# Optimization experiments

Hardware: AMD Instinct MI355X
Metric: run time of the kernel (lower is better)

## Reference

```python
import jax, jax.numpy as jnp
import numpy as np

DIM = 512
HEADS = 1
DIM_HEAD = DIM // 8          # 64
M = DIM // 2                 # 256 landmarks
ITERS = 6                    # pinv iterations
SCALE = DIM_HEAD ** -0.5
KSIZE = 33                   # residual conv kernel (seq dim)
EPS_LN = 1e-5


def setup_inputs() -> dict:
    key = jax.random.key(0)
    ks = jax.random.split(key, 6)
    B, N = 4, 4096  # N multiple of M -> no padding branch
    return {
        "x": jax.random.normal(ks[0], (B, N, DIM), jnp.float32),
        "norm_gamma": jnp.ones((DIM,), jnp.float32),
        "norm_beta": jnp.zeros((DIM,), jnp.float32),
        "w_qkv": jax.random.normal(ks[1], (DIM, 3 * HEADS * DIM_HEAD), jnp.float32) * 0.02,
        "w_out": jax.random.normal(ks[2], (HEADS * DIM_HEAD, DIM), jnp.float32) * 0.02,
        "b_out": jnp.zeros((DIM,), jnp.float32),
        "w_conv": jax.random.normal(ks[3], (HEADS, 1, KSIZE, 1), jnp.float32) * 0.02,
    }


def _moore_penrose_pinv(x, iters=ITERS):
    # x: [B, H, M, M]
    abs_x = jnp.abs(x)
    col = abs_x.sum(-1)
    row = abs_x.sum(-2)
    z = jnp.swapaxes(x, -1, -2) / (jnp.max(col) * jnp.max(row))  # global maxes, as in torch
    I = jnp.eye(x.shape[-1], dtype=x.dtype)
    for _ in range(iters):
        xz = x @ z
        z = 0.25 * z @ (13.0 * I - xz @ (15.0 * I - xz @ (7.0 * I - xz)))
    return z


def reference(x, norm_gamma, norm_beta, w_qkv, w_out, b_out, w_conv):
    B, N, _ = x.shape
    # LayerNorm (biased variance, matches torch)
    mu = x.mean(-1, keepdims=True)
    var = x.var(-1, keepdims=True)
    xn = (x - mu) / jnp.sqrt(var + EPS_LN) * norm_gamma + norm_beta

    qkv = xn @ w_qkv  # [B, N, 3*H*D]
    q, k, v = jnp.split(qkv, 3, axis=-1)
    resh = lambda t: t.reshape(B, N, HEADS, DIM_HEAD).transpose(0, 2, 1, 3)  # [B,H,N,D]
    q, k, v = resh(q), resh(k), resh(v)
    q = q * SCALE

    # landmarks: mean of l=N/M consecutive tokens
    l = N // M
    q_l = q.reshape(B, HEADS, M, l, DIM_HEAD).sum(3) / l  # [B,H,M,D]
    k_l = k.reshape(B, HEADS, M, l, DIM_HEAD).sum(3) / l

    sim1 = jnp.einsum('bhnd,bhmd->bhnm', q, k_l)    # [B,H,N,M]
    sim2 = jnp.einsum('bhid,bhjd->bhij', q_l, k_l)  # [B,H,M,M]
    sim3 = jnp.einsum('bhmd,bhnd->bhmn', q_l, k)    # [B,H,M,N]
    a1 = jax.nn.softmax(sim1, axis=-1)
    a2 = jax.nn.softmax(sim2, axis=-1)
    a3 = jax.nn.softmax(sim3, axis=-1)

    a2_inv = _moore_penrose_pinv(a2)
    left = a1 @ a2_inv                      # [B,H,N,M]
    out = left @ (a3 @ v)                   # [B,H,N,D]

    # residual depthwise conv over the sequence dim (treat [N,D] as HxW image)
    res = jax.lax.conv_general_dilated(
        v, w_conv, window_strides=(1, 1),
        padding=((KSIZE // 2, KSIZE // 2), (0, 0)),
        dimension_numbers=('NCHW', 'OIHW', 'NCHW'),
        feature_group_count=HEADS)
    out = out + res

    out = out.transpose(0, 2, 1, 3).reshape(B, N, HEADS * DIM_HEAD)
    out = out @ w_out + b_out               # to_out (dropout is eval no-op)

    attn = left @ a3                        # full approx attention [B,H,N,N]
    return (x + out, attn)
```

## Files before the change

### kernel.cpp

```cpp
#include <hip/hip_runtime.h>
#include <hip/hip_bf16.h>


typedef _Float16 f16;
typedef f16 f16x2 __attribute__((ext_vector_type(2)));
typedef f16 f16x4 __attribute__((ext_vector_type(4)));
typedef f16 f16x8 __attribute__((ext_vector_type(8)));
typedef float f32x4 __attribute__((ext_vector_type(4)));

__device__ __forceinline__ float waveMax(float v){
  #pragma unroll
  for(int i=32;i>0;i>>=1) v = fmaxf(v, __shfl_xor(v, i));
  return v;
}
__device__ __forceinline__ float waveSum(float v){
  #pragma unroll
  for(int i=32;i>0;i>>=1) v += __shfl_xor(v, i);
  return v;
}
__device__ __forceinline__ float blockMaxF(float v, float* sm){
  v = waveMax(v);
  if((threadIdx.x&63)==0) sm[threadIdx.x>>6] = v;
  __syncthreads();
  v = fmaxf(fmaxf(sm[0],sm[1]), fmaxf(sm[2],sm[3]));
  __syncthreads();
  return v;
}
__device__ __forceinline__ float blockSumF(float v, float* sm){
  v = waveSum(v);
  if((threadIdx.x&63)==0) sm[threadIdx.x>>6] = v;
  __syncthreads();
  v = sm[0]+sm[1]+sm[2]+sm[3];
  __syncthreads();
  return v;
}

__device__ __forceinline__ void async_cp16(const f16* g, const f16* l){
  __builtin_amdgcn_global_load_lds((const __attribute__((address_space(1))) void*)g,
                                   (__attribute__((address_space(3))) void*)l, 16, 0, 0);
}

__device__ __forceinline__ void gemm_body(
    const f16* __restrict__ A, const f16* __restrict__ Bt, void* __restrict__ C, int cf16,
    int N, int K, int m0, int n0, int kt0, int ktn,
    const float* __restrict__ bias, const float* __restrict__ resid,
    f16* As, f16* Bs)
{
  int t = threadIdx.x;
  int w = t>>6, lane = t&63;
  int quad = lane>>4, l16 = lane&15;
  int wr = w>>1, wc = w&1;
  f32x4 acc[4][4] = {};
  for(int kt=kt0; kt<kt0+ktn; ++kt){
    #pragma unroll
    for(int i=0;i<4;++i){
      int G = (w<<8)+(i<<6)+lane;
      int row = G>>3, gs = G&7;
      int g = gs ^ (row&7);
      int koff = (kt<<6)+(g<<3);
      async_cp16(A + (long)(m0+row)*K + koff, As + (((w<<8)+(i<<6))<<3));
      async_cp16(Bt + (long)(n0+row)*K + koff, Bs + (((w<<8)+(i<<6))<<3));
    }
    __syncthreads();
    #pragma unroll
    for(int kk=0; kk<2; ++kk){
      f16x8 af[4], bfr[4];
      int gb = (kk<<2) + quad;
      #pragma unroll
      for(int mi=0;mi<4;++mi){
        int row = (wr<<6)+(mi<<4)+l16;
        af[mi] = *(const f16x8*)(As + ((row<<6) + ((gb ^ (row&7))<<3)));
      }
      #pragma unroll
      for(int ni=0;ni<4;++ni){
        int row = (wc<<6)+(ni<<4)+l16;
        bfr[ni] = *(const f16x8*)(Bs + ((row<<6) + ((gb ^ (row&7))<<3)));
      }
      #pragma unroll
      for(int mi=0;mi<4;++mi){
        #pragma unroll
        for(int ni=0;ni<4;++ni)
          acc[mi][ni] = __builtin_amdgcn_mfma_f32_16x16x32_f16(af[mi], bfr[ni], acc[mi][ni], 0,0,0);
      }
    }
    __syncthreads();
  }
  #pragma unroll
  for(int mi=0;mi<4;++mi){
    int rowb = m0 + (wr<<6) + (mi<<4) + (quad<<2);
    #pragma unroll
    for(int ni=0;ni<4;++ni){
      int col = n0 + (wc<<6) + (ni<<4) + l16;
      if(col < N){
        #pragma unroll
        for(int r=0;r<4;++r){
          float v = acc[mi][ni][r];
          if(bias)  v += bias[col];
          if(resid) v += resid[(long)(rowb+r)*N + col];
          if(cf16) ((f16*)C)[(long)(rowb+r)*N + col] = (f16)v;
          else     ((float*)C)[(long)(rowb+r)*N + col] = v;
        }
      }
    }
  }
}

__device__ __forceinline__ void g256_body(const float* __restrict__ A, const float* __restrict__ B,
    const float* __restrict__ E, float* __restrict__ D, int Ncols, float beta, float alpha,
    int AS, int BS, int ES, int bx, int by, int b, int ks, float* At, float* Bss, float diagv)
{
  long aOff = (long)b*65536;
  long bBatch = 256L*Ncols, bSl = 4L*bBatch;
  long bOff = (long)b*bBatch;
  long dOff = (long)ks*bSl + bOff;
  int r0 = bx*64, c0 = by*64;
  int t = threadIdx.x, tr = t>>4, tc = t&15;
  int arow = t>>2, ac4 = t&3;
  int bk = t>>4, bn4 = t&15;
  float acc[4][4] = {};
  for(int k0=ks*64;k0<ks*64+64;k0+=16){
    const float* pa = A + aOff + (long)(r0+arow)*256 + k0 + ac4*4;
    float4 va = *(const float4*)pa;
    for(int s=1;s<AS;++s){ float4 w2 = *(const float4*)(pa + (long)s*262144);
      va.x+=w2.x; va.y+=w2.y; va.z+=w2.z; va.w+=w2.w; }
    At[(ac4*4+0)*72+arow]=va.x; At[(ac4*4+1)*72+arow]=va.y;
    At[(ac4*4+2)*72+arow]=va.z; At[(ac4*4+3)*72+arow]=va.w;
    const float* pb = B + bOff + (long)(k0+bk)*Ncols + c0 + bn4*4;
    float4 vb = *(const float4*)pb;
    for(int s=1;s<BS;++s){ float4 w2 = *(const float4*)(pb + (long)s*bSl);
      vb.x+=w2.x; vb.y+=w2.y; vb.z+=w2.z; vb.w+=w2.w; }
    *(float4*)&Bss[bk*72+bn4*4] = vb;
    __syncthreads();
    #pragma unroll
    for(int kk=0;kk<16;++kk){
      float4 a4 = *(const float4*)&At[kk*72+tr*4];
      float4 b4 = *(const float4*)&Bss[kk*72+tc*4];
      float av[4] = {a4.x,a4.y,a4.z,a4.w};
      float bv[4] = {b4.x,b4.y,b4.z,b4.w};
      #pragma unroll
      for(int i=0;i<4;++i){
        #pragma unroll
        for(int j=0;j<4;++j) acc[i][j] += av[i]*bv[j];
      }
    }
    __syncthreads();
  }
  #pragma unroll
  for(int i=0;i<4;++i){
    int row = r0 + tr*4 + i;
    #pragma unroll
    for(int j=0;j<4;++j){
      int col = c0 + tc*4 + j;
      float v = beta*acc[i][j];
      if(ks==0){
        if(ES>0){
          const float* pe = E + aOff + (long)row*256 + col;
          float e = pe[0];
          for(int s=1;s<ES;++s) e += pe[(long)s*262144];
          v += alpha*e;
        }
        if(row==col) v += diagv;
      }
      D[dOff + (long)row*Ncols + col] = v;
    }
  }
}

__global__ __launch_bounds__(256) void k_ln_prep(const float* __restrict__ x, const float* __restrict__ g,
    const float* __restrict__ be, f16* __restrict__ xn, const float* __restrict__ wqkv,
    const float* __restrict__ wout, f16* __restrict__ wqkT, f16* __restrict__ woutT,
    float* __restrict__ rs, unsigned* __restrict__ csmax){
  __shared__ float sm[8];
  int blk = blockIdx.x; int t = threadIdx.x;
  if(blk < 16384){
    long row = blk;
    const float* xr = x + row*512;
    float v0 = xr[t], v1 = xr[t+256];
    float s = waveSum(v0+v1), ss = waveSum(v0*v0+v1*v1);
    if((t&63)==0){ sm[t>>6] = s; sm[(t>>6)+4] = ss; }
    __syncthreads();
    s = sm[0]+sm[1]+sm[2]+sm[3]; ss = sm[4]+sm[5]+sm[6]+sm[7];
    float mu = s*(1.f/512.f);
    float var = ss*(1.f/512.f) - mu*mu;
    float rstd = rsqrtf(var + 1e-5f);
    xn[row*512+t]     = (f16)((v0-mu)*rstd*g[t]     + be[t]);
    xn[row*512+t+256] = (f16)((v1-mu)*rstd*g[t+256] + be[t+256]);
  } else if(blk < 16896){
    int i = (blk-16384)*256 + t; int n = i>>9, k = i&511;
    wqkT[i] = (n<192) ? (f16)wqkv[k*192+n] : (f16)0.0f;
  } else if(blk < 17024){
    int i = (blk-16896)*256 + t; int n = i>>6, k = i&63;
    woutT[i] = (f16)wout[k*512+n];
  } else {
    rs[t]=0.f; rs[t+256]=0.f; rs[t+512]=0.f; rs[t+768]=0.f;
    if(t==0){ *csmax = 0u; }
  }
}

__global__ __launch_bounds__(256) void k_qkv(const f16* __restrict__ xn, const f16* __restrict__ wqkT,
                                             float* __restrict__ qkv){
  __shared__ f16 As[8192];
  __shared__ f16 Bs[8192];
  int blk = blockIdx.x;
  int bx = blk&127, by = blk>>7;
  gemm_body(xn, wqkT, qkv, 0, 192, 512, bx*128, by*128, 0, 8, nullptr, nullptr, As, Bs);
}

__global__ __launch_bounds__(256) void k_splitvl(const float* __restrict__ qkv,
    f16* __restrict__ qf, f16* __restrict__ kf, float* __restrict__ vf,
    f16* __restrict__ vT, f16* __restrict__ ql, f16* __restrict__ kl){
  __shared__ float tile[64][65];
  int blk = blockIdx.x; int t = threadIdx.x;
  if(blk < 4096){
    long row = (long)blk*4 + (t>>6); int d = t&63;
    const float* p = qkv + row*192;
    qf[row*64+d] = (f16)(p[d]*0.125f);
    kf[row*64+d] = (f16)(p[d+64]);
    vf[row*64+d] = p[d+128];
  } else if(blk < 4352){
    int bidx = blk-4096; int b = bidx>>6, n0 = (bidx&63)*64;
    int c = t&63, r4 = t>>6;
    #pragma unroll
    for(int i=0;i<16;++i){ int r = i*4+r4;
      tile[r][c] = qkv[((long)(b*4096 + n0 + r))*192 + 128 + c]; }
    __syncthreads();
    #pragma unroll
    for(int i=0;i<16;++i){ int d = i*4+r4;
      vT[((long)(b*128 + d))*4096 + n0 + c] = (f16)tile[c][d]; }
  } else {
    int bidx = blk-4352;
    int bm = bidx*4 + (t>>6); int d = t&63;
    const float* p = qkv + (long)bm*16*192;
    float sq=0.f, sk=0.f;
    #pragma unroll
    for(int i=0;i<16;++i){ sq += p[i*192+d]; sk += p[i*192+64+d]; }
    ql[bm*64+d] = (f16)(sq*0.0625f*0.125f);
    kl[bm*64+d] = (f16)(sk*0.0625f);
  }
}

__global__ __launch_bounds__(256) void k_sims(const f16* __restrict__ qf, const f16* __restrict__ kf,
    const f16* __restrict__ ql, const f16* __restrict__ kl,
    float* __restrict__ s1, float* __restrict__ s2, float* __restrict__ s3){
  __shared__ f16 As[8192];
  __shared__ f16 Bs[8192];
  int blk = blockIdx.x;
  if(blk < 256){
    int bx = blk&31, by = (blk>>5)&1, b = blk>>6;
    gemm_body(qf + (long)b*262144, kl + (long)b*16384, s1 + (long)b*1048576, 0,
              256, 64, bx*128, by*128, 0, 1, nullptr, nullptr, As, Bs);
  } else if(blk < 272){
    int idx = blk-256;
    int bx = idx&1, by = (idx>>1)&1, b = idx>>2;
    gemm_body(ql + (long)b*16384, kl + (long)b*16384, s2 + (long)b*65536, 0,
              256, 64, bx*128, by*128, 0, 1, nullptr, nullptr, As, Bs);
  } else {
    int idx = blk-272;
    int bx = idx&1, by = (idx>>1)&31, b = idx>>6;
    gemm_body(ql + (long)b*16384, kf + (long)b*262144, s3 + (long)b*1048576, 0,
              4096, 64, bx*128, by*128, 0, 1, nullptr, nullptr, As, Bs);
  }
}

__global__ __launch_bounds__(256) void k_softmaxes(const float* __restrict__ s1, f16* __restrict__ a1,
    const float* __restrict__ s2, float* __restrict__ a2, float* __restrict__ rs, unsigned* __restrict__ csmax,
    const float* __restrict__ s3, f16* __restrict__ a3){
  __shared__ float sm[4];
  int blk = blockIdx.x; int t = threadIdx.x;
  if(blk < 4096){
    int w = t>>6, lane = t&63;
    long row = (long)blk*4 + w;
    float4 v = *(const float4*)(s1 + row*256 + lane*4);
    float m = waveMax(fmaxf(fmaxf(v.x,v.y),fmaxf(v.z,v.w)));
    float e0 = __expf(v.x-m), e1 = __expf(v.y-m), e2 = __expf(v.z-m), e3 = __expf(v.w-m);
    float inv = 1.f/waveSum(e0+e1+e2+e3);
    f16x4 o = {(f16)(e0*inv),(f16)(e1*inv),(f16)(e2*inv),(f16)(e3*inv)};
    *(f16x4*)(a1 + row*256 + lane*4) = o;
  } else if(blk < 5120){
    int row = blk-4096; int b = row>>8;
    float v = s2[row*256+t];
    float m = blockMaxF(v, sm);
    float e = __expf(v-m);
    float sum = blockSumF(e, sm);
    float p = e/sum;
    a2[(long)row*256+t] = p;
    atomicAdd(&rs[b*256+t], p);
    float rowsum = blockSumF(p, sm);
    if(t==0) atomicMax(csmax, __float_as_uint(rowsum));
  } else {
    long row = blk-5120;
    const float* p = s3 + row*4096;
    float4 v[4]; float m = -1e30f;
    #pragma unroll
    for(int i=0;i<4;++i){
      v[i] = *(const float4*)(p + (i*256+t)*4);
      m = fmaxf(m, fmaxf(fmaxf(v[i].x,v[i].y),fmaxf(v[i].z,v[i].w)));
    }
    m = blockMaxF(m, sm);
    float sum = 0.f;
    #pragma unroll
    for(int i=0;i<4;++i){
      v[i].x = __expf(v[i].x-m); v[i].y = __expf(v[i].y-m);
      v[i].z = __expf(v[i].z-m); v[i].w = __expf(v[i].w-m);
      sum += v[i].x+v[i].y+v[i].z+v[i].w;
    }
    float inv = 1.f/blockSumF(sum, sm);
    f16* o = a3 + row*4096;
    #pragma unroll
    for(int i=0;i<4;++i){
      f16x4 ov = {(f16)(v[i].x*inv),(f16)(v[i].y*inv),(f16)(v[i].z*inv),(f16)(v[i].w*inv)};
      *(f16x4*)(o + (i*256+t)*4) = ov;
    }
  }
}

__global__ __launch_bounds__(256) void k_z0(const float* __restrict__ a2, const float* __restrict__ rs,
                                            const unsigned* __restrict__ csmax, float* __restrict__ z){
  __shared__ float tile[64][65];
  __shared__ float sm[4];
  int b = blockIdx.z; int i0 = blockIdx.x*64, j0 = blockIdx.y*64;
  int t = threadIdx.x;
  float m = fmaxf(fmaxf(rs[t],rs[t+256]), fmaxf(rs[t+512],rs[t+768]));
  m = blockMaxF(m, sm);
  float sc = 1.f/(__uint_as_float(*csmax)*m);
  const float* A = a2 + (long)b*65536; float* Z = z + (long)b*65536;
  int c = t&63, r4 = t>>6;
  #pragma unroll
  for(int i=0;i<16;++i){ int r = i*4+r4; tile[r][c] = A[(j0+r)*256 + i0 + c]; }
  __syncthreads();
  #pragma unroll
  for(int i=0;i<16;++i){ int r = i*4+r4; Z[(i0+r)*256 + j0 + c] = tile[c][r]*sc; }
}

__global__ __launch_bounds__(256) void k_trA3_a3v(const f16* __restrict__ a3, f16* __restrict__ a3T,
    const f16* __restrict__ vT, float* __restrict__ a3vp){
  __shared__ f16 As[8192];
  __shared__ f16 Bs[8192];
  __shared__ f16 tile[64][74];
  int blk = blockIdx.x; int t = threadIdx.x;
  if(blk < 1024){
    int bx = blk&63, by = (blk>>6)&3, b = blk>>8;
    int n0 = bx*64, m0 = by*64;
    const f16* A = a3 + (long)b*1048576; f16* T = a3T + (long)b*1048576;
    int c = t&63, r4 = t>>6;
    #pragma unroll
    for(int i=0;i<16;++i){ int r = i*4+r4; tile[r][c] = A[(long)(m0+r)*4096 + n0 + c]; }
    __syncthreads();
    #pragma unroll
    for(int i=0;i<16;++i){ int nr = i*4+r4; T[(long)(n0+nr)*256 + m0 + c] = tile[c][nr]; }
  } else {
    int idx = blk-1024;
    int bx = idx&1, zz = idx>>1;
    int b = zz>>3, ksl = zz&7;
    gemm_body(a3 + (long)b*1048576, vT + (long)b*524288,
              a3vp + (long)ksl*65536 + (long)b*16384, 0,
              64, 4096, bx*128, 0, ksl*8, 8, nullptr, nullptr, As, Bs);
  }
}

__global__ __launch_bounds__(256) void k_g256(const float* __restrict__ A, const float* __restrict__ B,
    const float* __restrict__ E, float* __restrict__ D, float beta, float alpha,
    int AS, int BS, int ES, float diagv){
  __shared__ float At[1152];
  __shared__ float Bss[1152];
  int z = blockIdx.z; int b = z&3, ks = z>>2;
  g256_body(A, B, E, D, 256, beta, alpha, AS, BS, ES, blockIdx.x, blockIdx.y, b, ks, At, Bss, diagv);
}

__global__ __launch_bounds__(256) void k_nszy(const float* __restrict__ zc, int zAS,
    const float* __restrict__ y, const float* __restrict__ w3,
    float* __restrict__ zn, float* __restrict__ yn){
  __shared__ float At[1152];
  __shared__ float Bss[1152];
  int z = blockIdx.z;
  if(z < 16){
    int b = z&3, ks = z>>2;
    g256_body(zc, w3, nullptr, zn, 256, 0.25f, 0.f, zAS, 4, 0, blockIdx.x, blockIdx.y, b, ks, At, Bss, 0.f);
  } else {
    int zz = z-16; int b = zz&3, ks = zz>>2;
    g256_body(y, w3, nullptr, yn, 256, 0.25f, 0.f, 4, 4, 0, blockIdx.x, blockIdx.y, b, ks, At, Bss, 0.f);
  }
}

__global__ __launch_bounds__(256) void k_tail(const float* __restrict__ zc, const float* __restrict__ a3vp,
    float* __restrict__ pW, f16* __restrict__ zb){
  __shared__ float At[1152];
  __shared__ float Bss[1152];
  int blk = blockIdx.x; int t = threadIdx.x;
  if(blk < 64){
    int zx = blk&3, zz = blk>>2;
    int b = zz&3, ks = zz>>2;
    g256_body(zc, a3vp, nullptr, pW, 64, 1.f, 0.f, 4, 8, 0, zx, 0, b, ks, At, Bss, 0.f);
  } else if(blk < 192){
    int base = (blk-64)*2048;
    #pragma unroll
    for(int k=0;k<8;++k){
      int i = base + k*256 + t;
      float v = zc[i] + zc[i+262144] + zc[i+524288] + zc[i+786432];
      zb[i] = (f16)v;
    }
  }
}

__global__ __launch_bounds__(256) void k_trZ(const float* __restrict__ pW, f16* __restrict__ zaT){
  int i = blockIdx.x*256 + threadIdx.x;
  int b = i>>15, j = i&32767; int d = j>>8, m = j&255;
  float v = 0.f;
  if(d<64){
    long base = (long)b*16384 + (long)m*64 + d;
    v = pW[base] + pW[base+65536] + pW[base+131072] + pW[base+196608];
  }
  zaT[i] = (f16)v;
}

__global__ __launch_bounds__(256) void k_outh_U(const f16* __restrict__ a1, const f16* __restrict__ zaT,
    float* __restrict__ outh, const f16* __restrict__ a3T, const f16* __restrict__ zb, f16* __restrict__ U){
  __shared__ f16 As[8192];
  __shared__ f16 Bs[8192];
  int blk = blockIdx.x;
  if(blk < 128){
    int bx = blk&31, b = blk>>5;
    gemm_body(a1 + (long)b*1048576, zaT + (long)b*32768, outh + (long)b*262144, 0,
              64, 256, bx*128, 0, 0, 4, nullptr, nullptr, As, Bs);
  } else {
    int idx = blk-128;
    int bx = idx&31, by = (idx>>5)&1, b = idx>>6;
    gemm_body(a3T + (long)b*1048576, zb + (long)b*65536, U + (long)b*1048576, 1,
              256, 256, bx*128, by*128, 0, 4, nullptr, nullptr, As, Bs);
  }
}

__global__ __launch_bounds__(256) void k_h(const float* __restrict__ outh, const float* __restrict__ vf,
                                           const float* __restrict__ wconv, f16* __restrict__ h){
  __shared__ float wc[33];
  if(threadIdx.x<33) wc[threadIdx.x]=wconv[threadIdx.x];
  __syncthreads();
  long e = (long)blockIdx.x*256 + threadIdx.x;
  int d = (int)(e&63); long row = e>>6; int n = (int)(row&4095); long brow = row - n;
  float acc = outh[e];
  #pragma unroll
  for(int tau=0;tau<33;++tau){
    int nn = n + tau - 16;
    if(nn>=0 && nn<4096) acc += wc[tau]*vf[(brow+nn)*64 + d];
  }
  h[e] = (f16)acc;
}

__global__ __launch_bounds__(256) void k_out_attn(const f16* __restrict__ h, const f16* __restrict__ woutT,
    const float* __restrict__ x, const float* __restrict__ bout, float* __restrict__ out0,
    const f16* __restrict__ a1, const f16* __restrict__ U, float* __restrict__ attn){
  __shared__ f16 As[8192];
  __shared__ f16 Bs[8192];
  int blk = blockIdx.x;
  if(blk < 512){
    int bx = blk&127, by = blk>>7;
    gemm_body(h, woutT, out0, 0, 512, 64, bx*128, by*128, 0, 1, bout, x, As, Bs);
  } else {
    int idx = blk-512;
    int bx = idx&31, by = (idx>>5)&31, b = idx>>10;
    gemm_body(a1 + (long)b*1048576, U + (long)b*1048576, attn + (long)b*16777216, 0,
              4096, 256, bx*128, by*128, 0, 4, nullptr, nullptr, As, Bs);
  }
}

extern "C" void kernel_launch(void* const* d_in, const int* in_sizes, int n_in,
                              void* d_out, int out_size, void* d_ws, size_t ws_size,
                              hipStream_t stream) {
  (void)in_sizes; (void)n_in; (void)out_size; (void)ws_size;
  const float* x     = (const float*)d_in[0];
  const float* gamma = (const float*)d_in[1];
  const float* beta  = (const float*)d_in[2];
  const float* wqkv  = (const float*)d_in[3];
  const float* wout  = (const float*)d_in[4];
  const float* bout  = (const float*)d_in[5];
  const float* wconv = (const float*)d_in[6];

  char* ws = (char*)d_ws;
  f16*   xn   = (f16*)(ws + 0);
  float* s3   = (float*)(ws + 0);
  float* s1   = (float*)(ws + 16777216);
  f16*   a3T  = (f16*)(ws + 16777216);
  f16*   U    = (f16*)(ws + 25165824);
  float* qkv  = (float*)(ws + 33554432);
  f16*   a3   = (f16*)(ws + 33554432);
  f16*   a1   = (f16*)(ws + 46137344);
  f16*   qf   = (f16*)(ws + 54525952);
  f16*   kf   = (f16*)(ws + 56623104);
  float* vf   = (float*)(ws + 58720256);
  f16*   vT   = (f16*)(ws + 62914560);
  f16*   wqkT = (f16*)(ws + 67108864);
  f16*   ql   = (f16*)(ws + 67371008);
  f16*   kl   = (f16*)(ws + 67502080);
  float* s2   = (float*)(ws + 67633152);
  float* a2   = (float*)(ws + 68681728);
  float* zA   = (float*)(ws + 69730304);
  f16*   zb   = (f16*)(ws + 74973184);
  float* rs   = (float*)(ws + 76021760);
  unsigned* csmax = (unsigned*)(ws + 76021760 + 4096);
  f16*   zaT  = (f16*)(ws + 76029952);
  f16*   woutT= (f16*)(ws + 76292096);
  float* outh = (float*)(ws + 76357632);
  f16*   h    = (f16*)(ws + 80551936);
  float* pXZ  = (float*)(ws + 82649088);
  float* pT1  = (float*)(ws + 86843392);
  float* pT2  = (float*)(ws + 91037696);
  float* pU0  = (float*)(ws + 95232000);
  float* pU1  = (float*)(ws + 99426304);
  float* a3vp = (float*)(ws + 103620608);
  float* pW   = (float*)(ws + 105717760);

  float* out0 = (float*)d_out;
  float* attn = out0 + 8388608;

  k_ln_prep<<<17025,256,0,stream>>>(x, gamma, beta, xn, wqkv, wout, wqkT, woutT, rs, csmax);
  k_qkv<<<256,256,0,stream>>>(xn, wqkT, qkv);
  k_splitvl<<<4608,256,0,stream>>>(qkv, qf, kf, vf, vT, ql, kl);
  k_sims<<<528,256,0,stream>>>(qf, kf, ql, kl, s1, s2, s3);
  k_softmaxes<<<6144,256,0,stream>>>(s1, a1, s2, a2, rs, csmax, s3, a3);
  k_z0<<<dim3(4,4,4),256,0,stream>>>(a2, rs, csmax, zA);
  k_trA3_a3v<<<1088,256,0,stream>>>(a3, a3T, vT, a3vp);

  float* yb = pXZ;
  float* wb = pT1;
  k_g256<<<dim3(4,4,16),256,0,stream>>>(a2, zA, nullptr, yb, 1.f, 0.f, 1, 1, 0, 0.f);
  const float* zc = zA; int zAS = 1;
  for(int it=0; it<6; ++it){
    k_g256<<<dim3(4,4,16),256,0,stream>>>(yb, yb, yb, wb, 1.f, -7.f, 4, 4, 4, 15.f);
    k_g256<<<dim3(4,4,16),256,0,stream>>>(yb, wb, nullptr, pT2, -1.f, 0.f, 4, 4, 0, 13.f);
    float* zn = (it&1) ? pU1 : pU0;
    if(it < 5){
      k_nszy<<<dim3(4,4,32),256,0,stream>>>(zc, zAS, yb, pT2, zn, wb);
      float* tmp = yb; yb = wb; wb = tmp;
    } else {
      k_nszy<<<dim3(4,4,16),256,0,stream>>>(zc, zAS, yb, pT2, zn, wb);
    }
    zc = zn; zAS = 4;
  }
  k_tail<<<192,256,0,stream>>>(zc, a3vp, pW, zb);
  k_trZ<<<512,256,0,stream>>>(pW, zaT);

  k_outh_U<<<384,256,0,stream>>>(a1, zaT, outh, a3T, zb, U);
  k_h<<<4096,256,0,stream>>>(outh, vf, wconv, h);
  k_out_attn<<<4608,256,0,stream>>>(h, woutT, x, bout, out0, a1, U, attn);
}
```

Measured before the change: 751.8 us.

## Restructure pinv iterations into two launches and fuse conv residual into outh GEMM

The Newton-Schulz step is re-expressed algebraically. Each iteration now computes y² and z·y in one launch, then builds the polynomial terms inside the B-operand load of a second launch, so three launches per iteration become two. The initial z0 transpose and y0 = a2·a2ᵀ·scale are merged into one kernel. The depthwise residual conv is folded into the a1·zaT GEMM epilogue through shared memory, which removes the k_h launch and the outh round trip. The cost is extra B2 partial-sum loads in every tile and a larger LDS footprint for the outh kernel.

```diff
diff --git a/kernel.cpp b/kernel.cpp
--- a/kernel.cpp
+++ b/kernel.cpp
@@ -106,6 +106,7 @@
 }
 
 __device__ __forceinline__ void g256_body(const float* __restrict__ A, const float* __restrict__ B,
+    const float* __restrict__ B2, float cB2, float diagB,
     const float* __restrict__ E, float* __restrict__ D, int Ncols, float beta, float alpha,
     int AS, int BS, int ES, int bx, int by, int b, int ks, float* At, float* Bss, float diagv)
 {
@@ -129,6 +130,18 @@
     float4 vb = *(const float4*)pb;
     for(int s=1;s<BS;++s){ float4 w2 = *(const float4*)(pb + (long)s*bSl);
       vb.x+=w2.x; vb.y+=w2.y; vb.z+=w2.z; vb.w+=w2.w; }
+    if(B2){
+      const float* pb2 = B2 + (long)b*65536 + (long)(k0+bk)*256 + c0 + bn4*4;
+      float s2x=0.f,s2y=0.f,s2z=0.f,s2w=0.f;
+      for(int s=0;s<4;++s){ float4 w2 = *(const float4*)(pb2 + (long)s*262144);
+        s2x+=w2.x; s2y+=w2.y; s2z+=w2.z; s2w+=w2.w; }
+      vb.x+=cB2*s2x; vb.y+=cB2*s2y; vb.z+=cB2*s2z; vb.w+=cB2*s2w;
+    }
+    if(diagB != 0.f){
+      int kglob = k0 + bk, cbase = c0 + bn4*4;
+      float* pv = &vb.x;
+      if(kglob>=cbase && kglob<cbase+4) pv[kglob-cbase] += diagB;
+    }
     *(float4*)&Bss[bk*72+bn4*4] = vb;
     __syncthreads();
     #pragma unroll
@@ -162,6 +175,48 @@
         if(row==col) v += diagv;
       }
       D[dOff + (long)row*Ncols + col] = v;
+    }
+  }
+}
+
+__device__ __forceinline__ void g256_aat(const float* __restrict__ A, float* __restrict__ D,
+    float sc, int bx, int by, int b, int ks, float* At, float* Bss)
+{
+  long aOff = (long)b*65536;
+  long dOff = (long)ks*1048576 + (long)b*65536;
+  int r0 = bx*64, c0 = by*64;
+  int t = threadIdx.x, tr = t>>4, tc = t&15;
+  int arow = t>>2, ac4 = t&3;
+  float acc[4][4] = {};
+  for(int k0=ks*64;k0<ks*64+64;k0+=16){
+    float4 va = *(const float4*)(A + aOff + (long)(r0+arow)*256 + k0 + ac4*4);
+    At[(ac4*4+0)*72+arow]=va.x; At[(ac4*4+1)*72+arow]=va.y;
+    At[(ac4*4+2)*72+arow]=va.z; At[(ac4*4+3)*72+arow]=va.w;
+    float4 vb = *(const float4*)(A + aOff + (long)(c0+arow)*256 + k0 + ac4*4);
+    Bss[(ac4*4+0)*72+arow]=vb.x; Bss[(ac4*4+1)*72+arow]=vb.y;
+    Bss[(ac4*4+2)*72+arow]=vb.z; Bss[(ac4*4+3)*72+arow]=vb.w;
+    __syncthreads();
+    #pragma unroll
+    for(int kk=0;kk<16;++kk){
+      float4 a4 = *(const float4*)&At[kk*72+tr*4];
+      float4 b4 = *(const float4*)&Bss[kk*72+tc*4];
+      float av[4] = {a4.x,a4.y,a4.z,a4.w};
+      float bv[4] = {b4.x,b4.y,b4.z,b4.w};
+      #pragma unroll
+      for(int i=0;i<4;++i){
+        #pragma unroll
+        for(int j=0;j<4;++j) acc[i][j] += av[i]*bv[j];
+      }
+    }
+    __syncthreads();
+  }
+  #pragma unroll
+  for(int i=0;i<4;++i){
+    int row = r0 + tr*4 + i;
+    #pragma unroll
+    for(int j=0;j<4;++j){
+      int col = c0 + tc*4 + j;
+      D[dOff + (long)row*256 + col] = sc*acc[i][j];
     }
   }
 }
@@ -314,24 +369,6 @@
   }
 }
 
-__global__ __launch_bounds__(256) void k_z0(const float* __restrict__ a2, const float* __restrict__ rs,
-                                            const unsigned* __restrict__ csmax, float* __restrict__ z){
-  __shared__ float tile[64][65];
-  __shared__ float sm[4];
-  int b = blockIdx.z; int i0 = blockIdx.x*64, j0 = blockIdx.y*64;
-  int t = threadIdx.x;
-  float m = fmaxf(fmaxf(rs[t],rs[t+256]), fmaxf(rs[t+512],rs[t+768]));
-  m = blockMaxF(m, sm);
-  float sc = 1.f/(__uint_as_float(*csmax)*m);
-  const float* A = a2 + (long)b*65536; float* Z = z + (long)b*65536;
-  int c = t&63, r4 = t>>6;
-  #pragma unroll
-  for(int i=0;i<16;++i){ int r = i*4+r4; tile[r][c] = A[(j0+r)*256 + i0 + c]; }
-  __syncthreads();
-  #pragma unroll
-  for(int i=0;i<16;++i){ int r = i*4+r4; Z[(i0+r)*256 + j0 + c] = tile[c][r]*sc; }
-}
-
 __global__ __launch_bounds__(256) void k_trA3_a3v(const f16* __restrict__ a3, f16* __restrict__ a3T,
     const f16* __restrict__ vT, float* __restrict__ a3vp){
   __shared__ f16 As[8192];
@@ -358,27 +395,63 @@
   }
 }
 
-__global__ __launch_bounds__(256) void k_g256(const float* __restrict__ A, const float* __restrict__ B,
-    const float* __restrict__ E, float* __restrict__ D, float beta, float alpha,
-    int AS, int BS, int ES, float diagv){
+__global__ __launch_bounds__(256) void k_z0y0(const float* __restrict__ a2, const float* __restrict__ rs,
+    const unsigned* __restrict__ csmax, float* __restrict__ zA, float* __restrict__ y0){
+  __shared__ float sm4[4];
   __shared__ float At[1152];
   __shared__ float Bss[1152];
-  int z = blockIdx.z; int b = z&3, ks = z>>2;
-  g256_body(A, B, E, D, 256, beta, alpha, AS, BS, ES, blockIdx.x, blockIdx.y, b, ks, At, Bss, diagv);
-}
-
-__global__ __launch_bounds__(256) void k_nszy(const float* __restrict__ zc, int zAS,
-    const float* __restrict__ y, const float* __restrict__ w3,
+  __shared__ float tile[64][65];
+  int blk = blockIdx.x; int t = threadIdx.x;
+  float m = fmaxf(fmaxf(rs[t],rs[t+256]), fmaxf(rs[t+512],rs[t+768]));
+  m = blockMaxF(m, sm4);
+  float sc = 1.f/(__uint_as_float(*csmax)*m);
+  if(blk < 64){
+    int ix = blk&3, jy = (blk>>2)&3, b = blk>>4;
+    int i0 = ix*64, j0 = jy*64;
+    const float* A = a2 + (long)b*65536; float* Z = zA + (long)b*65536;
+    int c = t&63, r4 = t>>6;
+    #pragma unroll
+    for(int i=0;i<16;++i){ int r = i*4+r4; tile[r][c] = A[(j0+r)*256 + i0 + c]; }
+    __syncthreads();
+    #pragma unroll
+    for(int i=0;i<16;++i){ int r = i*4+r4; Z[(i0+r)*256 + j0 + c] = tile[c][r]*sc; }
+  } else {
+    int idx = blk-64;
+    int bx = idx&3, by = (idx>>2)&3, b = (idx>>4)&3, ks = idx>>6;
+    g256_aat(a2, y0, sc, bx, by, b, ks, At, Bss);
+  }
+}
+
+__global__ __launch_bounds__(256) void k_nsA(const float* __restrict__ zc, int zAS,
+    const float* __restrict__ y, float* __restrict__ y2, float* __restrict__ u){
+  __shared__ float At[1152];
+  __shared__ float Bss[1152];
+  int z = blockIdx.z;
+  if(z < 16){
+    int b = z&3, ks = z>>2;
+    g256_body(y, y, nullptr, 0.f, 0.f, nullptr, y2, 256, 1.f, 0.f, 4, 4, 0,
+              blockIdx.x, blockIdx.y, b, ks, At, Bss, 0.f);
+  } else {
+    int zz = z-16; int b = zz&3, ks = zz>>2;
+    g256_body(zc, y, nullptr, 0.f, 0.f, nullptr, u, 256, 1.f, 0.f, zAS, 4, 0,
+              blockIdx.x, blockIdx.y, b, ks, At, Bss, 0.f);
+  }
+}
+
+__global__ __launch_bounds__(256) void k_nsB(const float* __restrict__ zc, int zAS,
+    const float* __restrict__ y, const float* __restrict__ y2, const float* __restrict__ u,
     float* __restrict__ zn, float* __restrict__ yn){
   __shared__ float At[1152];
   __shared__ float Bss[1152];
   int z = blockIdx.z;
   if(z < 16){
     int b = z&3, ks = z>>2;
-    g256_body(zc, w3, nullptr, zn, 256, 0.25f, 0.f, zAS, 4, 0, blockIdx.x, blockIdx.y, b, ks, At, Bss, 0.f);
+    g256_body(u, y2, y, -7.f, 15.f, zc, zn, 256, -0.25f, 3.25f, 4, 4, zAS,
+              blockIdx.x, blockIdx.y, b, ks, At, Bss, 0.f);
   } else {
     int zz = z-16; int b = zz&3, ks = zz>>2;
-    g256_body(y, w3, nullptr, yn, 256, 0.25f, 0.f, 4, 4, 0, blockIdx.x, blockIdx.y, b, ks, At, Bss, 0.f);
+    g256_body(y2, y2, y, -7.f, 15.f, y, yn, 256, -0.25f, 3.25f, 4, 4, 4,
+              blockIdx.x, blockIdx.y, b, ks, At, Bss, 0.f);
   }
 }
 
@@ -390,7 +463,8 @@
   if(blk < 64){
     int zx = blk&3, zz = blk>>2;
     int b = zz&3, ks = zz>>2;
-    g256_body(zc, a3vp, nullptr, pW, 64, 1.f, 0.f, 4, 8, 0, zx, 0, b, ks, At, Bss, 0.f);
+    g256_body(zc, a3vp, nullptr, 0.f, 0.f, nullptr, pW, 64, 1.f, 0.f, 4, 8, 0,
+              zx, 0, b, ks, At, Bss, 0.f);
   } else if(blk < 192){
     int base = (blk-64)*2048;
     #pragma unroll
@@ -414,36 +488,37 @@
 }
 
 __global__ __launch_bounds__(256) void k_outh_U(const f16* __restrict__ a1, const f16* __restrict__ zaT,
-    float* __restrict__ outh, const f16* __restrict__ a3T, const f16* __restrict__ zb, f16* __restrict__ U){
+    const float* __restrict__ vf, const float* __restrict__ wconv, f16* __restrict__ h,
+    const f16* __restrict__ a3T, const f16* __restrict__ zb, f16* __restrict__ U){
   __shared__ f16 As[8192];
   __shared__ f16 Bs[8192];
-  int blk = blockIdx.x;
+  __shared__ float hs[8192];
+  __shared__ float wc[33];
+  int blk = blockIdx.x; int t = threadIdx.x;
   if(blk < 128){
+    if(t<33) wc[t] = wconv[t];
     int bx = blk&31, b = blk>>5;
-    gemm_body(a1 + (long)b*1048576, zaT + (long)b*32768, outh + (long)b*262144, 0,
-              64, 256, bx*128, 0, 0, 4, nullptr, nullptr, As, Bs);
+    int m0 = bx*128;
+    gemm_body(a1 + (long)b*1048576 + (long)m0*256, zaT + (long)b*32768, hs, 0,
+              64, 256, 0, 0, 0, 4, nullptr, nullptr, As, Bs);
+    __syncthreads();
+    #pragma unroll
+    for(int i=0;i<32;++i){
+      int e = i*256+t; int d = e&63; int r = e>>6; int n = m0+r;
+      float acc = hs[e];
+      #pragma unroll
+      for(int tau=0;tau<33;++tau){
+        int nn = n + tau - 16;
+        if(nn>=0 && nn<4096) acc += wc[tau]*vf[((long)b*4096+nn)*64 + d];
+      }
+      h[((long)b*4096+n)*64 + d] = (f16)acc;
+    }
   } else {
     int idx = blk-128;
     int bx = idx&31, by = (idx>>5)&1, b = idx>>6;
     gemm_body(a3T + (long)b*1048576, zb + (long)b*65536, U + (long)b*1048576, 1,
               256, 256, bx*128, by*128, 0, 4, nullptr, nullptr, As, Bs);
   }
-}
-
-__global__ __launch_bounds__(256) void k_h(const float* __restrict__ outh, const float* __restrict__ vf,
-                                           const float* __restrict__ wconv, f16* __restrict__ h){
-  __shared__ float wc[33];
-  if(threadIdx.x<33) wc[threadIdx.x]=wconv[threadIdx.x];
-  __syncthreads();
-  long e = (long)blockIdx.x*256 + threadIdx.x;
-  int d = (int)(e&63); long row = e>>6; int n = (int)(row&4095); long brow = row - n;
-  float acc = outh[e];
-  #pragma unroll
-  for(int tau=0;tau<33;++tau){
-    int nn = n + tau - 16;
-    if(nn>=0 && nn<4096) acc += wc[tau]*vf[(brow+nn)*64 + d];
-  }
-  h[e] = (f16)acc;
 }
 
 __global__ __launch_bounds__(256) void k_out_attn(const f16* __restrict__ h, const f16* __restrict__ woutT,
@@ -483,6 +558,7 @@
   f16*   U    = (f16*)(ws + 25165824);
   float* qkv  = (float*)(ws + 33554432);
   f16*   a3   = (f16*)(ws + 33554432);
+  float* pY   = (float*)(ws + 33554432);
   f16*   a1   = (f16*)(ws + 46137344);
   f16*   qf   = (f16*)(ws + 54525952);
   f16*   kf   = (f16*)(ws + 56623104);
@@ -499,7 +575,6 @@
   unsigned* csmax = (unsigned*)(ws + 76021760 + 4096);
   f16*   zaT  = (f16*)(ws + 76029952);
   f16*   woutT= (f16*)(ws + 76292096);
-  float* outh = (float*)(ws + 76357632);
   f16*   h    = (f16*)(ws + 80551936);
   float* pXZ  = (float*)(ws + 82649088);
   float* pT1  = (float*)(ws + 86843392);
@@ -517,29 +592,25 @@
   k_splitvl<<<4608,256,0,stream>>>(qkv, qf, kf, vf, vT, ql, kl);
   k_sims<<<528,256,0,stream>>>(qf, kf, ql, kl, s1, s2, s3);
   k_softmaxes<<<6144,256,0,stream>>>(s1, a1, s2, a2, rs, csmax, s3, a3);
-  k_z0<<<dim3(4,4,4),256,0,stream>>>(a2, rs, csmax, zA);
   k_trA3_a3v<<<1088,256,0,stream>>>(a3, a3T, vT, a3vp);
-
-  float* yb = pXZ;
-  float* wb = pT1;
-  k_g256<<<dim3(4,4,16),256,0,stream>>>(a2, zA, nullptr, yb, 1.f, 0.f, 1, 1, 0, 0.f);
+  k_z0y0<<<320,256,0,stream>>>(a2, rs, csmax, zA, pXZ);
+
+  float* yb = pXZ;  float* yp = pY;
   const float* zc = zA; int zAS = 1;
   for(int it=0; it<6; ++it){
-    k_g256<<<dim3(4,4,16),256,0,stream>>>(yb, yb, yb, wb, 1.f, -7.f, 4, 4, 4, 15.f);
-    k_g256<<<dim3(4,4,16),256,0,stream>>>(yb, wb, nullptr, pT2, -1.f, 0.f, 4, 4, 0, 13.f);
+    k_nsA<<<dim3(4,4,32),256,0,stream>>>(zc, zAS, yb, pT1, pT2);
     float* zn = (it&1) ? pU1 : pU0;
     if(it < 5){
-      k_nszy<<<dim3(4,4,32),256,0,stream>>>(zc, zAS, yb, pT2, zn, wb);
-      float* tmp = yb; yb = wb; wb = tmp;
+      k_nsB<<<dim3(4,4,32),256,0,stream>>>(zc, zAS, yb, pT1, pT2, zn, yp);
+      float* tmp = yb; yb = yp; yp = tmp;
     } else {
-      k_nszy<<<dim3(4,4,16),256,0,stream>>>(zc, zAS, yb, pT2, zn, wb);
+      k_nsB<<<dim3(4,4,16),256,0,stream>>>(zc, zAS, yb, pT1, pT2, zn, yp);
     }
     zc = zn; zAS = 4;
   }
   k_tail<<<192,256,0,stream>>>(zc, a3vp, pW, zb);
   k_trZ<<<512,256,0,stream>>>(pW, zaT);
 
-  k_outh_U<<<384,256,0,stream>>>(a1, zaT, outh, a3T, zb, U);
-  k_h<<<4096,256,0,stream>>>(outh, vf, wconv, h);
+  k_outh_U<<<384,256,0,stream>>>(a1, zaT, vf, wconv, h, a3T, zb, U);
   k_out_attn<<<4608,256,0,stream>>>(h, woutT, x, bout, out0, a1, U, attn);
 }
```

New measurement: 1.531 ms. 2.04x slower.
